# Kernel optimization log

Hardware: AMD Instinct MI355X
Metric: run time of the kernel (lower is better)

The kernel has to match this reference:

```python
import jax, jax.numpy as jnp
import numpy as np

B, L, C, PS, K, NL, NH, DFF, MAXLEN = 64, 4096, 32, 16, 1024, 4, 8, 2048, 512
D = PS * C          # code_dim = 512
P = L // PS         # num_patches = 256
PA_H = 4            # heads in PatchCrossAttention (largest of {4,2,1} dividing C)
COMMIT = 0.25


def _ln(x, g, b, eps=1e-5):
    m = x.mean(-1, keepdims=True)
    v = x.var(-1, keepdims=True)
    return (x - m) / jnp.sqrt(v + eps) * g + b


def _mha(q, k, v, w_in, b_in, w_out, b_out, nh, mask=None):
    # torch nn.MultiheadAttention math: in_proj weight [3d, d], y = x @ W.T + b
    d = q.shape[-1]
    dh = d // nh
    wq, wk, wv = jnp.split(w_in, 3, axis=0)
    bq, bk, bv = jnp.split(b_in, 3, axis=0)
    qh = (q @ wq.T + bq).reshape(q.shape[0], q.shape[1], nh, dh)
    kh = (k @ wk.T + bk).reshape(k.shape[0], k.shape[1], nh, dh)
    vh = (v @ wv.T + bv).reshape(v.shape[0], v.shape[1], nh, dh)
    scores = jnp.einsum('bqhd,bkhd->bhqk', qh, kh) / jnp.sqrt(jnp.asarray(dh, q.dtype))
    if mask is not None:
        scores = jnp.where(mask, jnp.asarray(-jnp.inf, scores.dtype), scores)
    a = jax.nn.softmax(scores, axis=-1)
    o = jnp.einsum('bhqk,bkhd->bqhd', a, vh).reshape(q.shape[0], q.shape[1], d)
    return o @ w_out.T + b_out


def _forward(x, pa_lq, pa_pos, pa_win, pa_bin, pa_wout, pa_bout,
             pa_ln1g, pa_ln1b, pa_ln2g, pa_ln2b, pa_w1, pa_b1, pa_w2, pa_b2,
             cb, tf_pos, tf_win, tf_bin, tf_wout, tf_bout,
             tf_ln1g, tf_ln1b, tf_ln2g, tf_ln2b,
             tf_w1, tf_b1, tf_w2, tf_b2, fin_g, fin_b):
    Bx = x.shape[0]
    # --- patchify: [B, L, C] -> [B*P, PS, C] ---
    xp = x.reshape(Bx * P, PS, C)
    # --- PatchCrossAttention ---
    x_pos = xp + pa_pos                       # pos emb over patch steps
    lq = jnp.broadcast_to(pa_lq, xp.shape)    # learnable query tokens
    attn = _mha(lq, x_pos, x_pos, pa_win, pa_bin, pa_wout, pa_bout, PA_H)
    xn = _ln(lq + attn, pa_ln1g, pa_ln1b)
    f = jax.nn.gelu(xn @ pa_w1 + pa_b1, approximate=False) @ pa_w2 + pa_b2
    xo = _ln(xn + f, pa_ln2g, pa_ln2b)
    enc = xp + xo                             # residual to raw patch
    # --- flatten + VQ ---
    z = enc.reshape(Bx * P, D)
    d2 = (z * z).sum(1, keepdims=True) + (cb * cb).sum(1) - 2.0 * (z @ cb.T)
    idx = jnp.argmin(d2, axis=1)
    q = cb[idx]
    sg = jax.lax.stop_gradient
    e_loss = jnp.mean((sg(q) - z) ** 2)
    q_loss = jnp.mean((q - sg(z)) ** 2)
    vq_loss = q_loss + COMMIT * e_loss
    quant = z + sg(q - z)                     # straight-through
    # --- causal transformer over code sequence [B, P, D] ---
    t = quant.reshape(Bx, P, D) + tf_pos[:P]
    causal = jnp.triu(jnp.ones((P, P), dtype=bool), 1)
    for i in range(NL):  # post-LN TransformerEncoderLayer, gelu
        a = _mha(t, t, t, tf_win[i], tf_bin[i], tf_wout[i], tf_bout[i], NH, causal)
        t = _ln(t + a, tf_ln1g[i], tf_ln1b[i])
        f = jax.nn.gelu(t @ tf_w1[i] + tf_b1[i], approximate=False) @ tf_w2[i] + tf_b2[i]
        t = _ln(t + f, tf_ln2g[i], tf_ln2b[i])
    y = _ln(t, fin_g, fin_b)
    return y, vq_loss, idx


def setup_inputs() -> dict:
    key = jax.random.key(0)
    ks = iter(jax.random.split(key, 32))
    n = lambda shape, s=0.02: jax.random.normal(next(ks), shape, dtype=jnp.float32) * s
    inp = {
        'x': jax.random.normal(next(ks), (B, L, C), dtype=jnp.float32),
        'pa_lq': n((PS, C)), 'pa_pos': n((PS, C)),
        'pa_win': n((3 * C, C)), 'pa_bin': jnp.zeros((3 * C,), jnp.float32),
        'pa_wout': n((C, C)), 'pa_bout': jnp.zeros((C,), jnp.float32),
        'pa_ln1g': jnp.ones((C,), jnp.float32), 'pa_ln1b': jnp.zeros((C,), jnp.float32),
        'pa_ln2g': jnp.ones((C,), jnp.float32), 'pa_ln2b': jnp.zeros((C,), jnp.float32),
        'pa_w1': n((C, 2 * C)), 'pa_b1': jnp.zeros((2 * C,), jnp.float32),
        'pa_w2': n((2 * C, C)), 'pa_b2': jnp.zeros((C,), jnp.float32),
        'cb': jax.random.uniform(next(ks), (K, D), jnp.float32, -1.0 / K, 1.0 / K),
        'tf_pos': n((MAXLEN, D)),
        'tf_win': n((NL, 3 * D, D)), 'tf_bin': jnp.zeros((NL, 3 * D), jnp.float32),
        'tf_wout': n((NL, D, D)), 'tf_bout': jnp.zeros((NL, D), jnp.float32),
        'tf_ln1g': jnp.ones((NL, D), jnp.float32), 'tf_ln1b': jnp.zeros((NL, D), jnp.float32),
        'tf_ln2g': jnp.ones((NL, D), jnp.float32), 'tf_ln2b': jnp.zeros((NL, D), jnp.float32),
        'tf_w1': n((NL, D, DFF)), 'tf_b1': jnp.zeros((NL, DFF), jnp.float32),
        'tf_w2': n((NL, DFF, D)), 'tf_b2': jnp.zeros((NL, D), jnp.float32),
        'fin_g': jnp.ones((D,), jnp.float32), 'fin_b': jnp.zeros((D,), jnp.float32),
    }
    return inp


def reference(x, pa_lq, pa_pos, pa_win, pa_bin, pa_wout, pa_bout,
              pa_ln1g, pa_ln1b, pa_ln2g, pa_ln2b, pa_w1, pa_b1, pa_w2, pa_b2,
              cb, tf_pos, tf_win, tf_bin, tf_wout, tf_bout,
              tf_ln1g, tf_ln1b, tf_ln2g, tf_ln2b,
              tf_w1, tf_b1, tf_w2, tf_b2, fin_g, fin_b):
    return _forward(x, pa_lq, pa_pos, pa_win, pa_bin, pa_wout, pa_bout,
                    pa_ln1g, pa_ln1b, pa_ln2g, pa_ln2b, pa_w1, pa_b1, pa_w2, pa_b2,
                    cb, tf_pos, tf_win, tf_bin, tf_wout, tf_bout,
                    tf_ln1g, tf_ln1b, tf_ln2g, tf_ln2b,
                    tf_w1, tf_b1, tf_w2, tf_b2, fin_g, fin_b)
```

## Files before the change

### kernel.cpp

```cpp
#include <hip/hip_runtime.h>


#define SQRT1_2F 0.70710678118654752440f

typedef __attribute__((ext_vector_type(8))) short short8;
typedef __attribute__((ext_vector_type(4))) float f32x4;
typedef __attribute__((ext_vector_type(8))) unsigned short ushort8;
typedef unsigned short ushort;
typedef unsigned long long u64;

__device__ __forceinline__ float gelu_exact(float v) {
  return 0.5f * v * (1.0f + erff(v * SQRT1_2F));
}

__device__ __forceinline__ ushort f2b_rne(float f) {
  unsigned u = __float_as_uint(f);
  unsigned r = (u + 0x7fffu + ((u >> 16) & 1u)) >> 16;
  return (ushort)r;
}

__device__ __forceinline__ float b2f(ushort u) {
  return __uint_as_float(((unsigned)u) << 16);
}

__device__ __forceinline__ void gload16(const void* g, void* l) {
  __builtin_amdgcn_global_load_lds(
      (const __attribute__((address_space(1))) void*)g,
      (__attribute__((address_space(3))) void*)l, 16, 0, 0);
}

__device__ __forceinline__ unsigned fkey(float d) {
  unsigned u = __float_as_uint(d);
  return (u & 0x80000000u) ? ~u : (u | 0x80000000u);
}

__global__ __launch_bounds__(64) void patch_setup_kernel(
    const float* __restrict__ lq, const float* __restrict__ win,
    const float* __restrict__ bin, const float* __restrict__ w1,
    const float* __restrict__ w2, float* __restrict__ q16,
    float* __restrict__ w1T, float* __restrict__ w2T) {
  const int tid = threadIdx.x;
#pragma unroll
  for (int q = 0; q < 8; q++) {
    int e = tid + (q << 6);
    int i = e >> 5, c = e & 31;
    const float* wr = win + (size_t)c * 32;
    float acc = bin[c];
#pragma unroll
    for (int d = 0; d < 32; d++) acc += lq[(i << 5) + d] * wr[d];
    q16[e] = acc;
  }
#pragma unroll
  for (int q = 0; q < 32; q++) {
    int e = tid + (q << 6);
    int u = e >> 5, d = e & 31;
    w1T[e] = w1[(size_t)d * 64 + u];
  }
#pragma unroll
  for (int q = 0; q < 32; q++) {
    int e = tid + (q << 6);
    int c = e >> 6, u = e & 63;
    w2T[e] = w2[(size_t)u * 32 + c];
  }
}

__device__ __forceinline__ void ln_16xS(float* buf, const float* g,
                                        const float* bb, int tid) {
  int row = tid >> 2, sub = tid & 3;
  int c0 = sub << 3;
  float* r = buf + row * 34 + c0;
  float v[8];
  float s = 0.f, s2 = 0.f;
#pragma unroll
  for (int n = 0; n < 8; n++) {
    float t = r[n];
    v[n] = t; s += t; s2 += t * t;
  }
  s += __shfl_xor(s, 1);  s += __shfl_xor(s, 2);
  s2 += __shfl_xor(s2, 1); s2 += __shfl_xor(s2, 2);
  float m = s * (1.0f / 32.0f);
  float var = s2 * (1.0f / 32.0f) - m * m;
  float inv = 1.0f / sqrtf(var + 1e-5f);
#pragma unroll
  for (int n = 0; n < 8; n++)
    r[n] = (v[n] - m) * inv * g[c0 + n] + bb[c0 + n];
}

__global__ __launch_bounds__(256) void pkA_kernel(
    const float* __restrict__ x, const float* __restrict__ pos,
    const float* __restrict__ win, const float* __restrict__ bin,
    const float* __restrict__ q16, float* __restrict__ so) {
  __shared__ float sxp[2048];
  __shared__ float skv[4096];
  __shared__ float sq16[16 * 33];
  const int blk = blockIdx.x, t = threadIdx.x;
  const int p0 = blk << 2;
  const int cfix = t & 31;

#pragma unroll
  for (int q = 0; q < 8; q++) {
    int e = t + (q << 8);
    int pl = e >> 9, r = e & 511;
    sxp[e] = x[(size_t)(p0 + pl) * 512 + r] + pos[r];
  }
  if (t < 128) {
#pragma unroll
    for (int q = 0; q < 4; q++) {
      int e = t + (q << 7);
      sq16[(e >> 5) * 33 + (e & 31)] = q16[e];
    }
  }

  float wr0[32], wr1[32];
#pragma unroll
  for (int d4 = 0; d4 < 8; d4++) {
    *(float4*)(wr0 + 4 * d4) =
        *(const float4*)(win + (size_t)(32 + cfix) * 32 + 4 * d4);
    *(float4*)(wr1 + 4 * d4) =
        *(const float4*)(win + (size_t)(64 + cfix) * 32 + 4 * d4);
  }
  const float bk = bin[32 + cfix];
  const float bv = bin[64 + cfix];
  __syncthreads();

#pragma unroll
  for (int q = 0; q < 16; q++) {
    int e = t + (q << 8);
    int pl = e >> 10, rr = e & 1023;
    int w = rr >> 9, rj = rr & 511, j = rj >> 5;
    const float* sx = sxp + (pl << 9) + (j << 5);
    const float* wreg = w ? wr1 : wr0;
    float acc = w ? bv : bk;
#pragma unroll
    for (int d = 0; d < 32; d++) acc += sx[d] * wreg[d];
    skv[e] = acc;
  }
  __syncthreads();

  const int pl = t >> 6, hh = (t >> 4) & 3, i = t & 15;
  const int p = p0 + pl;
  const float* kp = skv + (pl << 10);
  const int hd = hh << 3;

  float sc[16];
#pragma unroll
  for (int j = 0; j < 16; j++) {
    float acc = 0.f;
#pragma unroll
    for (int d = 0; d < 8; d++)
      acc += sq16[i * 33 + hd + d] * kp[(j << 5) + hd + d];
    sc[j] = acc * 0.35355339059327373f;
  }
  {
    float mx = sc[0];
#pragma unroll
    for (int j = 1; j < 16; j++) mx = fmaxf(mx, sc[j]);
    float sm = 0.f;
    float ev[16];
#pragma unroll
    for (int j = 0; j < 16; j++) { ev[j] = expf(sc[j] - mx); sm += ev[j]; }
    float inv = 1.0f / sm;
#pragma unroll
    for (int j = 0; j < 16; j++) sc[j] = ev[j] * inv;
  }
  float* orow = so + (size_t)p * 512 + (i << 5) + hd;
#pragma unroll
  for (int c8 = 0; c8 < 8; c8++) {
    const int c = hd + c8;
    float acc = 0.f;
#pragma unroll
    for (int j = 0; j < 16; j++) acc += sc[j] * kp[512 + (j << 5) + c];
    orow[c8] = acc;
  }
}

__global__ __launch_bounds__(64) void pkB_kernel(
    const float* __restrict__ so_g, const float* __restrict__ x,
    const float* __restrict__ wout, const float* __restrict__ bout,
    const float* __restrict__ lq,
    const float* __restrict__ ln1g, const float* __restrict__ ln1b,
    const float* __restrict__ w1T, const float* __restrict__ b1,
    const float* __restrict__ w2T, const float* __restrict__ b2,
    const float* __restrict__ ln2g, const float* __restrict__ ln2b,
    float* __restrict__ z, ushort* __restrict__ zh,
    ushort* __restrict__ zl, float* __restrict__ znorm) {
  __shared__ float sso[544], sst[544], ssh[1056];
  const int p = blockIdx.x, t = threadIdx.x;
  const int cfix = t & 31;

#pragma unroll
  for (int q = 0; q < 8; q++) {
    int e = t + (q << 6);
    sso[(e >> 5) * 34 + (e & 31)] = so_g[(size_t)p * 512 + e];
  }

  float wo[32];
#pragma unroll
  for (int d4 = 0; d4 < 8; d4++)
    *(float4*)(wo + 4 * d4) = *(const float4*)(wout + (size_t)cfix * 32 + 4 * d4);
  __syncthreads();

#pragma unroll
  for (int q = 0; q < 8; q++) {
    int e = t + (q << 6);
    int i = e >> 5;
    float acc = bout[cfix];
#pragma unroll
    for (int d = 0; d < 32; d++) acc += sso[i * 34 + d] * wo[d];
    sst[i * 34 + cfix] = acc + lq[(i << 5) + cfix];
  }
  __syncthreads();
  ln_16xS(sst, ln1g, ln1b, t);

  float w1r[32];
#pragma unroll
  for (int d4 = 0; d4 < 8; d4++)
    *(float4*)(w1r + 4 * d4) = *(const float4*)(w1T + (size_t)t * 32 + 4 * d4);
  __syncthreads();

#pragma unroll
  for (int q = 0; q < 16; q++) {
    int i = q;
    float acc = b1[t];
#pragma unroll
    for (int d = 0; d < 32; d++) acc += sst[i * 34 + d] * w1r[d];
    ssh[i * 66 + t] = gelu_exact(acc);
  }

  float w2r[64];
#pragma unroll
  for (int u4 = 0; u4 < 16; u4++)
    *(float4*)(w2r + 4 * u4) = *(const float4*)(w2T + (size_t)cfix * 64 + 4 * u4);
  __syncthreads();

#pragma unroll
  for (int q = 0; q < 8; q++) {
    int e = t + (q << 6);
    int i = e >> 5;
    float acc = b2[cfix];
#pragma unroll
    for (int u = 0; u < 64; u++) acc += ssh[i * 66 + u] * w2r[u];
    sso[i * 34 + cfix] = acc + sst[i * 34 + cfix];
  }
  __syncthreads();
  ln_16xS(sso, ln2g, ln2b, t);
  __syncthreads();

  const float* xp = x + (size_t)p * 512;
  const int row = t >> 2, c0v = (t & 3) << 3;
  float zv[8];
#pragma unroll
  for (int n = 0; n < 8; n++)
    zv[n] = xp[(t << 3) + n] + sso[row * 34 + c0v + n];
  float* zo = z + (size_t)p * 512 + (t << 3);
  *(float4*)(zo)     = *(float4*)(zv);
  *(float4*)(zo + 4) = *(float4*)(zv + 4);
  ushort8 hv, lv;
  float s2 = 0.f;
#pragma unroll
  for (int n = 0; n < 8; n++) {
    s2 += zv[n] * zv[n];
    ushort h = f2b_rne(zv[n]);
    hv[n] = h;
    lv[n] = f2b_rne(zv[n] - b2f(h));
  }
  *(ushort8*)(zh + (size_t)p * 512 + (t << 3)) = hv;
  *(ushort8*)(zl + (size_t)p * 512 + (t << 3)) = lv;
#pragma unroll
  for (int off = 1; off < 64; off <<= 1) s2 += __shfl_xor(s2, off);
  if (t == 0) znorm[p] = s2;
}

__global__ __launch_bounds__(64) void cbnorm_kernel(
    const float* __restrict__ cb, float* __restrict__ cbn,
    ushort* __restrict__ ch, ushort* __restrict__ cl) {
  int c = blockIdx.x, lane = threadIdx.x;
  const float* r = cb + (size_t)c * 512 + lane * 8;
  float v[8];
  *(float4*)(v)     = *(const float4*)(r);
  *(float4*)(v + 4) = *(const float4*)(r + 4);
  float s = 0.f;
  ushort8 hv, lv;
#pragma unroll
  for (int n = 0; n < 8; n++) {
    s += v[n] * v[n];
    ushort h = f2b_rne(v[n]);
    hv[n] = h;
    lv[n] = f2b_rne(v[n] - b2f(h));
  }
  *(ushort8*)(ch + (size_t)c * 512 + lane * 8) = hv;
  *(ushort8*)(cl + (size_t)c * 512 + lane * 8) = lv;
#pragma unroll
  for (int off = 1; off < 64; off <<= 1) s += __shfl_xor(s, off);
  if (lane == 0) cbn[c] = s;
}

__global__ __launch_bounds__(256) void gemm_vq_b3(
    const ushort* __restrict__ Ah, const ushort* __restrict__ Al,
    const ushort* __restrict__ Bh, const ushort* __restrict__ Bl,
    const float* __restrict__ znorm, const float* __restrict__ cbn,
    u64* __restrict__ packed) {
  __shared__ ushort sAh[4096], sAl[4096], sBh[4096], sBl[4096];
  const int cpx = gridDim.x >> 3;
  const int bid = (blockIdx.x & 7) * cpx + (blockIdx.x >> 3);
  const int bx = bid & 7, by = bid >> 3;
  const int m0 = by << 7, n0 = bx << 7;
  const int tid = threadIdx.x;
  const int wid = tid >> 6, lane = tid & 63;
  const int wr = wid >> 1, wc = wid & 1;
  const int l15 = lane & 15, lk = lane >> 4;

  const f32x4 fzero = {0.f, 0.f, 0.f, 0.f};
  f32x4 acc[4][4];
#pragma unroll
  for (int i = 0; i < 4; i++)
#pragma unroll
    for (int j = 0; j < 4; j++) acc[i][j] = fzero;

  for (int k0 = 0; k0 < 512; k0 += 32) {
#pragma unroll
    for (int c = 0; c < 2; c++) {
      const int I = tid + (c << 8);
      const int r = I >> 2, kk = (I & 3) << 3;
      const size_t ga = (size_t)(m0 + r) * 512 + k0 + kk;
      const size_t gb = (size_t)(n0 + r) * 512 + k0 + kk;
      const size_t lo = (size_t)((wid << 6) + (c << 8)) * 8;
      gload16(Ah + ga, sAh + lo);
      gload16(Al + ga, sAl + lo);
      gload16(Bh + gb, sBh + lo);
      gload16(Bl + gb, sBl + lo);
    }
    __syncthreads();

    short8 ah[4], al[4], bh[4], bl[4];
#pragma unroll
    for (int m = 0; m < 4; m++) {
      const int ar = ((wr << 6) + (m << 4) + l15) * 32 + lk * 8;
      ah[m] = *(const short8*)(sAh + ar);
      al[m] = *(const short8*)(sAl + ar);
      const int br = ((wc << 6) + (m << 4) + l15) * 32 + lk * 8;
      bh[m] = *(const short8*)(sBh + br);
      bl[m] = *(const short8*)(sBl + br);
    }
#pragma unroll
    for (int m = 0; m < 4; m++)
#pragma unroll
      for (int n = 0; n < 4; n++) {
        acc[m][n] = __builtin_amdgcn_mfma_f32_16x16x32_bf16(ah[m], bh[n],
                                                            acc[m][n], 0, 0, 0);
        acc[m][n] = __builtin_amdgcn_mfma_f32_16x16x32_bf16(ah[m], bl[n],
                                                            acc[m][n], 0, 0, 0);
        acc[m][n] = __builtin_amdgcn_mfma_f32_16x16x32_bf16(al[m], bh[n],
                                                            acc[m][n], 0, 0, 0);
      }
    __syncthreads();
  }

  float zn[4][4];
#pragma unroll
  for (int m = 0; m < 4; m++)
#pragma unroll
    for (int r = 0; r < 4; r++)
      zn[m][r] = znorm[m0 + (wr << 6) + (m << 4) + (lk << 2) + r];
  float cbnv[4];
#pragma unroll
  for (int n = 0; n < 4; n++)
    cbnv[n] = cbn[n0 + (wc << 6) + (n << 4) + l15];

#pragma unroll
  for (int m = 0; m < 4; m++) {
#pragma unroll
    for (int r = 0; r < 4; r++) {
      u64 best = ~0ull;
#pragma unroll
      for (int n = 0; n < 4; n++) {
        const int gcol = n0 + (wc << 6) + (n << 4) + l15;
        float d = (zn[m][r] + cbnv[n]) - 2.0f * acc[m][n][r];
        u64 key = ((u64)fkey(d) << 32) | (unsigned)gcol;
        best = best < key ? best : key;
      }
#pragma unroll
      for (int off = 1; off < 16; off <<= 1) {
        u64 o = __shfl_xor(best, off);
        best = best < o ? best : o;
      }
      if (l15 == 0) {
        const int grow = m0 + (wr << 6) + (m << 4) + (lk << 2) + r;
        atomicMin(&packed[grow], best);
      }
    }
  }
}

__global__ __launch_bounds__(256) void vq_slim_kernel(
    const u64* __restrict__ packed, const float* __restrict__ cb,
    const float* __restrict__ z, const float* __restrict__ tf_pos,
    float* __restrict__ t, ushort* __restrict__ th,
    float* __restrict__ idx_out, float* __restrict__ loss_part) {
  __shared__ float spart[4];
  const int wv = threadIdx.x >> 6;
  const int r = (blockIdx.x << 2) + wv;
  const int lane = threadIdx.x & 63;
  const int bi = (int)(unsigned)(packed[r] & 0xFFFFFFFFull);
  const float* zr = z + (size_t)r * 512 + (lane << 3);
  const float* q = cb + (size_t)bi * 512 + (lane << 3);
  const float* pr = tf_pos + (size_t)(r & 255) * 512 + (lane << 3);
  float zv[8], qv[8], pv[8];
  *(float4*)(zv)     = *(const float4*)(zr);
  *(float4*)(zv + 4) = *(const float4*)(zr + 4);
  *(float4*)(qv)     = *(const float4*)(q);
  *(float4*)(qv + 4) = *(const float4*)(q + 4);
  *(float4*)(pv)     = *(const float4*)(pr);
  *(float4*)(pv + 4) = *(const float4*)(pr + 4);
  float lsum = 0.f;
  float tv[8];
  ushort8 w;
#pragma unroll
  for (int n = 0; n < 8; n++) {
    float diff = qv[n] - zv[n];
    lsum += diff * diff;
    tv[n] = qv[n] + pv[n];
    w[n] = f2b_rne(tv[n]);
  }
  float* to = t + (size_t)r * 512 + (lane << 3);
  *(float4*)(to)     = *(float4*)(tv);
  *(float4*)(to + 4) = *(float4*)(tv + 4);
  *(ushort8*)(th + (size_t)r * 512 + (lane << 3)) = w;
#pragma unroll
  for (int off = 1; off < 64; off <<= 1) lsum += __shfl_xor(lsum, off);
  if (lane == 0) {
    idx_out[r] = (float)bi;
    spart[wv] = lsum;
  }
  __syncthreads();
  if (threadIdx.x == 0)
    loss_part[blockIdx.x] = (spart[0] + spart[1]) + (spart[2] + spart[3]);
}

__global__ __launch_bounds__(256) void loss_reduce_kernel(
    const float* __restrict__ loss_part, float* __restrict__ loss_out) {
  __shared__ float sw[4];
  float s = 0.f;
  for (int i = threadIdx.x; i < 4096; i += 256) s += loss_part[i];
#pragma unroll
  for (int off = 1; off < 64; off <<= 1) s += __shfl_xor(s, off);
  const int wv = threadIdx.x >> 6;
  if ((threadIdx.x & 63) == 0) sw[wv] = s;
  __syncthreads();
  if (threadIdx.x == 0)
    loss_out[0] = ((sw[0] + sw[1]) + (sw[2] + sw[3])) * (1.25f / 8388608.0f);
}

template <int OUTMODE>
__global__ __launch_bounds__(256) void gemm_bf16_kernel(
    const ushort* __restrict__ A, const ushort* __restrict__ B,
    const float* __restrict__ bias, void* __restrict__ Cout,
    int M, int N, int K) {
  __shared__ ushort As[4096];
  __shared__ ushort Bs[4096];
  const int nbx = N >> 7;
  const int cpx = gridDim.x >> 3;
  const int bid = (blockIdx.x & 7) * cpx + (blockIdx.x >> 3);
  const int bx = bid % nbx, by = bid / nbx;
  const int m0 = by << 7, n0 = bx << 7;
  const int tid = threadIdx.x;
  const int wid = tid >> 6, lane = tid & 63;
  const int wr = wid >> 1, wc = wid & 1;
  const int l15 = lane & 15, lk = lane >> 4;

  const f32x4 fzero = {0.f, 0.f, 0.f, 0.f};
  f32x4 acc[4][4];
#pragma unroll
  for (int i = 0; i < 4; i++)
#pragma unroll
    for (int j = 0; j < 4; j++) acc[i][j] = fzero;

  for (int k0 = 0; k0 < K; k0 += 32) {
#pragma unroll
    for (int c = 0; c < 2; c++) {
      const int I = tid + (c << 8);
      const int r = I >> 2, kk = (I & 3) << 3;
      gload16(A + (size_t)(m0 + r) * K + k0 + kk,
              As + (size_t)((wid << 6) + (c << 8)) * 8);
      gload16(B + (size_t)(n0 + r) * K + k0 + kk,
              Bs + (size_t)((wid << 6) + (c << 8)) * 8);
    }
    __syncthreads();

    short8 a[4], b[4];
#pragma unroll
    for (int m = 0; m < 4; m++) {
      const int ar = (wr << 6) + (m << 4) + l15;
      a[m] = *(const short8*)(As + ar * 32 + lk * 8);
      const int br = (wc << 6) + (m << 4) + l15;
      b[m] = *(const short8*)(Bs + br * 32 + lk * 8);
    }
#pragma unroll
    for (int m = 0; m < 4; m++)
#pragma unroll
      for (int n = 0; n < 4; n++)
        acc[m][n] = __builtin_amdgcn_mfma_f32_16x16x32_bf16(a[m], b[n],
                                                            acc[m][n], 0, 0, 0);
    __syncthreads();
  }

  float bv[4];
#pragma unroll
  for (int n = 0; n < 4; n++)
    bv[n] = bias[n0 + (wc << 6) + (n << 4) + l15];

#pragma unroll
  for (int m = 0; m < 4; m++) {
#pragma unroll
    for (int n = 0; n < 4; n++) {
      const int gcol = n0 + (wc << 6) + (n << 4) + l15;
#pragma unroll
      for (int r = 0; r < 4; r++) {
        const int grow = m0 + (wr << 6) + (m << 4) + (lk << 2) + r;
        float v = acc[m][n][r] + bv[n];
        if (OUTMODE == 0) {
          ((float*)Cout)[(size_t)grow * N + gcol] = v;
        } else if (OUTMODE == 1) {
          ((ushort*)Cout)[(size_t)grow * N + gcol] = f2b_rne(gelu_exact(v));
        } else {
          ((ushort*)Cout)[(size_t)grow * N + gcol] = f2b_rne(v);
        }
      }
    }
  }
}

__global__ void cvt_flat(const float* __restrict__ in, ushort* __restrict__ out,
                         int n) {
  int i = blockIdx.x * blockDim.x + threadIdx.x;
  const int stride = gridDim.x * blockDim.x;
  for (; i < n; i += stride) out[i] = f2b_rne(in[i]);
}

__global__ __launch_bounds__(256) void cvt_tr(const float* __restrict__ in,
                                              ushort* __restrict__ out,
                                              int R, int C) {
  __shared__ float tile[32][33];
  const int bc = blockIdx.x, br = blockIdx.y, lay = blockIdx.z;
  const float* src = in + (size_t)lay * R * C;
  ushort* dst = out + (size_t)lay * R * C;
  const int tid = threadIdx.x;
#pragma unroll
  for (int q = 0; q < 4; q++) {
    int idx = tid + (q << 8);
    int rr = idx >> 5, cc = idx & 31;
    tile[rr][cc] = src[(size_t)(br * 32 + rr) * C + bc * 32 + cc];
  }
  __syncthreads();
#pragma unroll
  for (int q = 0; q < 4; q++) {
    int idx = tid + (q << 8);
    int co = idx >> 5, ro = idx & 31;
    dst[(size_t)(bc * 32 + co) * R + br * 32 + ro] = f2b_rne(tile[ro][co]);
  }
}

__global__ __launch_bounds__(64) void attn_mfma_kernel(
    const ushort* __restrict__ qkv, ushort* __restrict__ o) {
  __shared__ ushort lds[8192];
  char* KsB = (char*)lds;
  char* VtB = (char*)(lds + 4096);
  const int bid = blockIdx.x;
  const int xcd = bid & 7, slot = bid >> 3;
  const int b = (xcd << 3) | (slot >> 5);
  const int h = (slot >> 2) & 7;
  const int qb = slot & 3;
  const int lane = threadIdx.x;
  const int l15 = lane & 15, lk4 = lane >> 4;

  short8 qf[4][2];
#pragma unroll
  for (int m = 0; m < 4; m++)
#pragma unroll
    for (int kc = 0; kc < 2; kc++)
      qf[m][kc] = *(const short8*)(qkv +
          (size_t)(b * 256 + qb * 64 + m * 16 + l15) * 1536 +
          h * 64 + kc * 32 + lk4 * 8);

  const f32x4 fz = {0.f, 0.f, 0.f, 0.f};
  f32x4 O[4][4];
#pragma unroll
  for (int m = 0; m < 4; m++)
#pragma unroll
    for (int n = 0; n < 4; n++) O[m][n] = fz;
  float lsum[4][4];
#pragma unroll
  for (int m = 0; m < 4; m++)
#pragma unroll
    for (int r = 0; r < 4; r++) lsum[m][r] = 0.f;

  for (int jt = 0; jt <= qb; jt++) {
    ushort8 kv[8], vv[8];
    const ushort* krow = qkv + (size_t)(b * 256 + jt * 64 + lane) * 1536 +
                         512 + h * 64;
#pragma unroll
    for (int u = 0; u < 8; u++) kv[u] = ((const ushort8*)krow)[u];
#pragma unroll
    for (int u = 0; u < 8; u++) vv[u] = ((const ushort8*)(krow + 512))[u];
    __syncthreads();
    {
      const int rx = (lane & 7) << 4;
#pragma unroll
      for (int u = 0; u < 8; u++)
        *(ushort8*)(KsB + lane * 128 + ((u << 4) ^ rx)) = kv[u];
#pragma unroll
      for (int u = 0; u < 8; u++)
#pragma unroll
        for (int i = 0; i < 8; i++) {
          const int d = u * 8 + i;
          *(ushort*)(VtB + ((d * 128 + lane * 2) ^ ((d & 7) << 4))) =
              (ushort)vv[u][i];
        }
    }
    __syncthreads();

    f32x4 sacc[4][4];
#pragma unroll
    for (int m = 0; m < 4; m++)
#pragma unroll
      for (int n = 0; n < 4; n++) sacc[m][n] = fz;
#pragma unroll
    for (int kc = 0; kc < 2; kc++) {
      short8 bf[4];
#pragma unroll
      for (int n = 0; n < 4; n++) {
        const int row = n * 16 + l15;
        bf[n] = *(const short8*)(KsB + row * 128 +
                                 ((kc * 64 + lk4 * 16) ^ ((row & 7) << 4)));
      }
#pragma unroll
      for (int m = 0; m < 4; m++)
#pragma unroll
        for (int n = 0; n < 4; n++)
          sacc[m][n] = __builtin_amdgcn_mfma_f32_16x16x32_bf16(
              qf[m][kc], bf[n], sacc[m][n], 0, 0, 0);
    }
    __syncthreads();

    const bool diag = (jt == qb);
#pragma unroll
    for (int m = 0; m < 4; m++)
#pragma unroll
      for (int n = 0; n < 4; n++)
#pragma unroll
        for (int r = 0; r < 4; r++) {
          const int ql = m * 16 + lk4 * 4 + r;
          const int jl = n * 16 + l15;
          float e = __expf(sacc[m][n][r] * 0.125f);
          if (diag && jl > ql) e = 0.f;
          const ushort pu = f2b_rne(e);
          lsum[m][r] += b2f(pu);
          *(ushort*)(KsB + ql * 128 + ((jl * 2) ^ ((ql & 7) << 4))) = pu;
        }
    __syncthreads();

#pragma unroll
    for (int kc = 0; kc < 2; kc++) {
      short8 pf[4], vf[4];
#pragma unroll
      for (int m = 0; m < 4; m++) {
        const int row = m * 16 + l15;
        pf[m] = *(const short8*)(KsB + row * 128 +
                                 ((kc * 64 + lk4 * 16) ^ ((row & 7) << 4)));
      }
#pragma unroll
      for (int n = 0; n < 4; n++) {
        const int row = n * 16 + l15;
        vf[n] = *(const short8*)(VtB + row * 128 +
                                 ((kc * 64 + lk4 * 16) ^ ((row & 7) << 4)));
      }
#pragma unroll
      for (int m = 0; m < 4; m++)
#pragma unroll
        for (int n = 0; n < 4; n++)
          O[m][n] = __builtin_amdgcn_mfma_f32_16x16x32_bf16(
              pf[m], vf[n], O[m][n], 0, 0, 0);
    }
  }

  float inv[4][4];
#pragma unroll
  for (int m = 0; m < 4; m++)
#pragma unroll
    for (int r = 0; r < 4; r++) {
      float v = lsum[m][r];
      v += __shfl_xor(v, 1); v += __shfl_xor(v, 2);
      v += __shfl_xor(v, 4); v += __shfl_xor(v, 8);
      inv[m][r] = 1.0f / v;
    }
#pragma unroll
  for (int m = 0; m < 4; m++)
#pragma unroll
    for (int n = 0; n < 4; n++)
#pragma unroll
      for (int r = 0; r < 4; r++) {
        const int row = b * 256 + qb * 64 + m * 16 + lk4 * 4 + r;
        const int col = h * 64 + n * 16 + l15;
        o[(size_t)row * 512 + col] = f2b_rne(O[m][n][r] * inv[m][r]);
      }
}

__global__ __launch_bounds__(256) void ln_kernel(
    const float* __restrict__ xin, const ushort* __restrict__ addin_b,
    const float* __restrict__ g, const float* __restrict__ bb,
    float* __restrict__ outp, ushort* __restrict__ outb) {
  const int r = blockIdx.x * 4 + (threadIdx.x >> 6);
  const int lane = threadIdx.x & 63;
  const float* xr = xin + (size_t)r * 512 + lane * 8;
  float v[8];
  *(float4*)(v)     = *(const float4*)(xr);
  *(float4*)(v + 4) = *(const float4*)(xr + 4);
  if (addin_b) {
    ushort8 a = *(const ushort8*)(addin_b + (size_t)r * 512 + lane * 8);
#pragma unroll
    for (int n = 0; n < 8; n++) v[n] += b2f(a[n]);
  }
  float s = 0.f, s2 = 0.f;
#pragma unroll
  for (int n = 0; n < 8; n++) { s += v[n]; s2 += v[n] * v[n]; }
#pragma unroll
  for (int off = 1; off < 64; off <<= 1) {
    s += __shfl_xor(s, off);
    s2 += __shfl_xor(s2, off);
  }
  float m = s * (1.0f / 512.0f);
  float var = s2 * (1.0f / 512.0f) - m * m;
  float inv = 1.0f / sqrtf(var + 1e-5f);
  const int c0 = lane * 8;
  float outv[8];
#pragma unroll
  for (int n = 0; n < 8; n++) outv[n] = (v[n] - m) * inv * g[c0 + n] + bb[c0 + n];
  float* orow = outp + (size_t)r * 512 + c0;
  *(float4*)(orow)     = *(float4*)(outv);
  *(float4*)(orow + 4) = *(float4*)(outv + 4);
  if (outb) {
    ushort8 w;
#pragma unroll
    for (int n = 0; n < 8; n++) w[n] = f2b_rne(outv[n]);
    *(ushort8*)(outb + (size_t)r * 512 + c0) = w;
  }
}

extern "C" void kernel_launch(void* const* d_in, const int* in_sizes, int n_in,
                              void* d_out, int out_size, void* d_ws, size_t ws_size,
                              hipStream_t stream) {
  const float* x       = (const float*)d_in[0];
  const float* pa_lq   = (const float*)d_in[1];
  const float* pa_pos  = (const float*)d_in[2];
  const float* pa_win  = (const float*)d_in[3];
  const float* pa_bin  = (const float*)d_in[4];
  const float* pa_wout = (const float*)d_in[5];
  const float* pa_bout = (const float*)d_in[6];
  const float* pa_ln1g = (const float*)d_in[7];
  const float* pa_ln1b = (const float*)d_in[8];
  const float* pa_ln2g = (const float*)d_in[9];
  const float* pa_ln2b = (const float*)d_in[10];
  const float* pa_w1   = (const float*)d_in[11];
  const float* pa_b1   = (const float*)d_in[12];
  const float* pa_w2   = (const float*)d_in[13];
  const float* pa_b2   = (const float*)d_in[14];
  const float* cb      = (const float*)d_in[15];
  const float* tf_pos  = (const float*)d_in[16];
  const float* tf_win  = (const float*)d_in[17];
  const float* tf_bin  = (const float*)d_in[18];
  const float* tf_wout = (const float*)d_in[19];
  const float* tf_bout = (const float*)d_in[20];
  const float* tf_ln1g = (const float*)d_in[21];
  const float* tf_ln1b = (const float*)d_in[22];
  const float* tf_ln2g = (const float*)d_in[23];
  const float* tf_ln2b = (const float*)d_in[24];
  const float* tf_w1   = (const float*)d_in[25];
  const float* tf_b1   = (const float*)d_in[26];
  const float* tf_w2   = (const float*)d_in[27];
  const float* tf_b2   = (const float*)d_in[28];
  const float* fin_g   = (const float*)d_in[29];
  const float* fin_b   = (const float*)d_in[30];

  float* yout = (float*)d_out;
  float* loss_out = yout + 8388608;
  float* idx_out = loss_out + 1;

  float* ws   = (float*)d_ws;
  float* z    = ws;
  float* tb   = z + 8388608;
  float* bufA = tb + 8388608;
  float* bufC = bufA + 16777216;
  float* wreg = bufC + 8388608;
  float* treg = wreg + 6291456;
  float* cbn  = treg + 4194304;
  float* q16  = cbn + 1024;
  float* w1T  = q16 + 512;
  float* w2T  = w1T + 2048;
  float* znorm = w2T + 2048;
  u64*   packed = (u64*)(znorm + 16384);
  float* loss_part = (float*)(packed + 16384);

  ushort* win_b  = (ushort*)wreg;
  ushort* wout_b = win_b + 3145728;
  ushort* w1t_b  = wout_b + 1048576;
  ushort* w2t_b  = w1t_b + 4194304;
  ushort* tbh    = (ushort*)treg;
  ushort* qkvh   = (ushort*)bufA;
  ushort* abh    = (ushort*)z;
  ushort* zh_b   = (ushort*)bufC;
  ushort* zl_b   = zh_b + 8388608;
  ushort* projh  = (ushort*)bufC;
  ushort* ch_b   = (ushort*)treg;
  ushort* cl_b   = ch_b + 524288;

  hipMemsetAsync(packed, 0xFF, 16384 * sizeof(u64), stream);
  cbnorm_kernel<<<1024, 64, 0, stream>>>(cb, cbn, ch_b, cl_b);
  patch_setup_kernel<<<1, 64, 0, stream>>>(pa_lq, pa_win, pa_bin, pa_w1,
                                           pa_w2, q16, w1T, w2T);

  pkA_kernel<<<4096, 256, 0, stream>>>(x, pa_pos, pa_win, pa_bin, q16, bufA);
  pkB_kernel<<<16384, 64, 0, stream>>>(bufA, x, pa_wout, pa_bout, pa_lq,
                                       pa_ln1g, pa_ln1b, w1T, pa_b1,
                                       w2T, pa_b2, pa_ln2g, pa_ln2b, z,
                                       zh_b, zl_b, znorm);

  cvt_flat<<<2048, 256, 0, stream>>>(tf_win, win_b, 3145728);
  cvt_flat<<<1024, 256, 0, stream>>>(tf_wout, wout_b, 1048576);
  cvt_tr<<<dim3(64, 16, 4), 256, 0, stream>>>(tf_w1, w1t_b, 512, 2048);
  cvt_tr<<<dim3(16, 64, 4), 256, 0, stream>>>(tf_w2, w2t_b, 2048, 512);

  gemm_vq_b3<<<dim3(1024), 256, 0, stream>>>(zh_b, zl_b, ch_b, cl_b,
                                             znorm, cbn, packed);
  vq_slim_kernel<<<4096, 256, 0, stream>>>(packed, cb, z, tf_pos, tb, tbh,
                                           idx_out, loss_part);
  loss_reduce_kernel<<<1, 256, 0, stream>>>(loss_part, loss_out);

  for (int l = 0; l < 4; l++) {
    gemm_bf16_kernel<2><<<dim3(128 * 12), 256, 0, stream>>>(
        tbh, win_b + (size_t)l * 1536 * 512, tf_bin + l * 1536, qkvh,
        16384, 1536, 512);
    attn_mfma_kernel<<<dim3(2048), 64, 0, stream>>>(qkvh, abh);
    gemm_bf16_kernel<2><<<dim3(128 * 4), 256, 0, stream>>>(
        abh, wout_b + (size_t)l * 512 * 512, tf_bout + l * 512, projh,
        16384, 512, 512);
    ln_kernel<<<dim3(4096), 256, 0, stream>>>(tb, projh, tf_ln1g + l * 512,
                                              tf_ln1b + l * 512, tb, tbh);
    gemm_bf16_kernel<1><<<dim3(128 * 16), 256, 0, stream>>>(
        tbh, w1t_b + (size_t)l * 1048576, tf_b1 + l * 2048, qkvh,
        16384, 2048, 512);
    gemm_bf16_kernel<2><<<dim3(128 * 4), 256, 0, stream>>>(
        qkvh, w2t_b + (size_t)l * 1048576, tf_b2 + l * 512, projh,
        16384, 512, 2048);
    ln_kernel<<<dim3(4096), 256, 0, stream>>>(tb, projh, tf_ln2g + l * 512,
                                              tf_ln2b + l * 512, tb, tbh);
  }
  ln_kernel<<<dim3(4096), 256, 0, stream>>>(tb, nullptr, fin_g, fin_b, yout,
                                            nullptr);

  (void)in_sizes; (void)n_in; (void)out_size; (void)ws_size;
}
```

Before: 1.369 ms.

## Double K-depth in bf16 GEMM and prefetch next K/V tile in attention

The bf16 GEMM now stages a 64-wide K slice per iteration (two 32-wide halves in doubled LDS buffers), which halves the number of barrier pairs per output tile. The causal attention kernel issues the global loads for the next K/V tile into registers right after the current tile is written to LDS, so those loads overlap with the QK and PV MFMA work. It also raises wave priority around the MFMA blocks. The cost is twice the LDS per GEMM block, which may lower occupancy, and more live registers in the attention loop.

```diff
diff --git a/kernel.cpp b/kernel.cpp
--- a/kernel.cpp
+++ b/kernel.cpp
@@ -456,8 +456,8 @@
     const ushort* __restrict__ A, const ushort* __restrict__ B,
     const float* __restrict__ bias, void* __restrict__ Cout,
     int M, int N, int K) {
-  __shared__ ushort As[4096];
-  __shared__ ushort Bs[4096];
+  __shared__ ushort As[8192];
+  __shared__ ushort Bs[8192];
   const int nbx = N >> 7;
   const int cpx = gridDim.x >> 3;
   const int bid = (blockIdx.x & 7) * cpx + (blockIdx.x >> 3);
@@ -475,32 +475,38 @@
 #pragma unroll
     for (int j = 0; j < 4; j++) acc[i][j] = fzero;
 
-  for (int k0 = 0; k0 < K; k0 += 32) {
-#pragma unroll
-    for (int c = 0; c < 2; c++) {
-      const int I = tid + (c << 8);
-      const int r = I >> 2, kk = (I & 3) << 3;
-      gload16(A + (size_t)(m0 + r) * K + k0 + kk,
-              As + (size_t)((wid << 6) + (c << 8)) * 8);
-      gload16(B + (size_t)(n0 + r) * K + k0 + kk,
-              Bs + (size_t)((wid << 6) + (c << 8)) * 8);
+  for (int k0 = 0; k0 < K; k0 += 64) {
+#pragma unroll
+    for (int c = 0; c < 4; c++) {
+      const int base = (c << 8) + (wid << 6);
+      const int half = base >> 9;
+      const int Jb = base & 511;
+      const int J = Jb + lane;
+      const int r = J >> 2, kk = (J & 3) << 3;
+      gload16(A + (size_t)(m0 + r) * K + k0 + (half << 5) + kk,
+              As + (size_t)((half << 12) + Jb * 8));
+      gload16(B + (size_t)(n0 + r) * K + k0 + (half << 5) + kk,
+              Bs + (size_t)((half << 12) + Jb * 8));
     }
     __syncthreads();
 
-    short8 a[4], b[4];
-#pragma unroll
-    for (int m = 0; m < 4; m++) {
-      const int ar = (wr << 6) + (m << 4) + l15;
-      a[m] = *(const short8*)(As + ar * 32 + lk * 8);
-      const int br = (wc << 6) + (m << 4) + l15;
-      b[m] = *(const short8*)(Bs + br * 32 + lk * 8);
-    }
-#pragma unroll
-    for (int m = 0; m < 4; m++)
-#pragma unroll
-      for (int n = 0; n < 4; n++)
-        acc[m][n] = __builtin_amdgcn_mfma_f32_16x16x32_bf16(a[m], b[n],
-                                                            acc[m][n], 0, 0, 0);
+#pragma unroll
+    for (int kc = 0; kc < 2; kc++) {
+      short8 a[4], b[4];
+#pragma unroll
+      for (int m = 0; m < 4; m++) {
+        const int ar = (kc << 12) + ((wr << 6) + (m << 4) + l15) * 32 + lk * 8;
+        a[m] = *(const short8*)(As + ar);
+        const int br = (kc << 12) + ((wc << 6) + (m << 4) + l15) * 32 + lk * 8;
+        b[m] = *(const short8*)(Bs + br);
+      }
+#pragma unroll
+      for (int m = 0; m < 4; m++)
+#pragma unroll
+        for (int n = 0; n < 4; n++)
+          acc[m][n] = __builtin_amdgcn_mfma_f32_16x16x32_bf16(a[m], b[n],
+                                                              acc[m][n], 0, 0, 0);
+    }
     __syncthreads();
   }
 
@@ -594,14 +600,16 @@
 #pragma unroll
     for (int r = 0; r < 4; r++) lsum[m][r] = 0.f;
 
+  ushort8 kv[8], vv[8];
+  {
+    const ushort* krow = qkv + (size_t)(b * 256 + lane) * 1536 + 512 + h * 64;
+#pragma unroll
+    for (int u = 0; u < 8; u++) kv[u] = ((const ushort8*)krow)[u];
+#pragma unroll
+    for (int u = 0; u < 8; u++) vv[u] = ((const ushort8*)(krow + 512))[u];
+  }
+
   for (int jt = 0; jt <= qb; jt++) {
-    ushort8 kv[8], vv[8];
-    const ushort* krow = qkv + (size_t)(b * 256 + jt * 64 + lane) * 1536 +
-                         512 + h * 64;
-#pragma unroll
-    for (int u = 0; u < 8; u++) kv[u] = ((const ushort8*)krow)[u];
-#pragma unroll
-    for (int u = 0; u < 8; u++) vv[u] = ((const ushort8*)(krow + 512))[u];
     __syncthreads();
     {
       const int rx = (lane & 7) << 4;
@@ -619,11 +627,21 @@
     }
     __syncthreads();
 
+    if (jt < qb) {
+      const ushort* krow = qkv +
+          (size_t)(b * 256 + (jt + 1) * 64 + lane) * 1536 + 512 + h * 64;
+#pragma unroll
+      for (int u = 0; u < 8; u++) kv[u] = ((const ushort8*)krow)[u];
+#pragma unroll
+      for (int u = 0; u < 8; u++) vv[u] = ((const ushort8*)(krow + 512))[u];
+    }
+
     f32x4 sacc[4][4];
 #pragma unroll
     for (int m = 0; m < 4; m++)
 #pragma unroll
       for (int n = 0; n < 4; n++) sacc[m][n] = fz;
+    __builtin_amdgcn_s_setprio(1);
 #pragma unroll
     for (int kc = 0; kc < 2; kc++) {
       short8 bf[4];
@@ -640,6 +658,7 @@
           sacc[m][n] = __builtin_amdgcn_mfma_f32_16x16x32_bf16(
               qf[m][kc], bf[n], sacc[m][n], 0, 0, 0);
     }
+    __builtin_amdgcn_s_setprio(0);
     __syncthreads();
 
     const bool diag = (jt == qb);
@@ -659,6 +678,7 @@
         }
     __syncthreads();
 
+    __builtin_amdgcn_s_setprio(1);
 #pragma unroll
     for (int kc = 0; kc < 2; kc++) {
       short8 pf[4], vf[4];
@@ -681,6 +701,7 @@
           O[m][n] = __builtin_amdgcn_mfma_f32_16x16x32_bf16(
               pf[m], vf[n], O[m][n], 0, 0, 0);
     }
+    __builtin_amdgcn_s_setprio(0);
   }
 
   float inv[4][4];
```

New measurement: 1.303 ms. 1.05x faster.
